# Performance work log

Hardware: AMD Instinct MI355X
Metric: run time of the kernel (lower is better)

Reference implementation:

```python
import jax, jax.numpy as jnp
import numpy as np

ALPHA = 0.1
B, N, M = 384, 256, 64
EPS = 1e-5


def _lsa(cost):
    """Exact linear sum assignment (Jonker-Volgenant shortest augmenting path).
    cost: (n, m) with n <= m. Returns col4row: for each row, its assigned column.
    Matches scipy.optimize.linear_sum_assignment.
    """
    cost = np.asarray(cost, dtype=np.float64)
    n, m = cost.shape
    u = np.zeros(n)
    v = np.zeros(m)
    col4row = np.full(n, -1, dtype=np.int64)
    row4col = np.full(m, -1, dtype=np.int64)
    for cur_row in range(n):
        min_val = 0.0
        i = cur_row
        SR = np.zeros(n, dtype=bool)
        SC = np.zeros(m, dtype=bool)
        shortest = np.full(m, np.inf)
        prev = np.full(m, -1, dtype=np.int64)
        sink = -1
        while sink == -1:
            SR[i] = True
            rem = ~SC
            cols = np.nonzero(rem)[0]
            d = min_val + cost[i, cols] - u[i] - v[cols]
            upd = d < shortest[cols]
            shortest[cols[upd]] = d[upd]
            prev[cols[upd]] = i
            j = int(np.argmin(np.where(SC, np.inf, shortest)))
            min_val = shortest[j]
            SC[j] = True
            if row4col[j] == -1:
                sink = j
            else:
                i = row4col[j]
        # dual updates
        u[cur_row] += min_val
        sr = SR.copy()
        sr[cur_row] = False
        rows = np.nonzero(sr)[0]
        u[rows] += min_val - shortest[col4row[rows]]
        scc = np.nonzero(SC)[0]
        v[scc] -= min_val - shortest[scc]
        # augment along the alternating path
        j = sink
        while True:
            i = prev[j]
            row4col[j] = i
            col4row[i], j = j, col4row[i]
            if i == cur_row:
                break
    return col4row


def _assignments(pred_np, label_np, lens_np):
    """Build the (detached) one-hot assignment tensor X[b, pred, label]."""
    conf = pred_np[..., 3]
    log_c = np.log(conf + EPS)
    log_ca = np.log(1.0 - conf + EPS)
    X = np.zeros((pred_np.shape[0], pred_np.shape[1], label_np.shape[1]), dtype=np.float32)
    for b in range(pred_np.shape[0]):
        L = int(lens_np[b])
        diff = pred_np[b, :, None, :3] - label_np[b, None, :L, :]   # [N, L, 3]
        nd = (diff * diff).sum(-1)                                  # [N, L]
        C = ALPHA * nd / 2.0 - log_c[b][:, None] + log_ca[b][:, None]
        matched_preds = _lsa(C.T)                                   # [L] distinct pred indices
        X[b, matched_preds, np.arange(L)] = 1.0
    return X


def setup_inputs() -> dict:
    key = jax.random.key(0)
    k1, k2, k3 = jax.random.split(key, 3)
    pred = jax.random.uniform(k1, (B, N, 4), dtype=jnp.float32)      # coords + confidence in (0,1)
    label = jax.random.uniform(k2, (B, M, 3), dtype=jnp.float32)
    label_len = jax.random.randint(k3, (B,), 1, M + 1, dtype=jnp.int32)
    return {"pred": pred, "label": label, "label_len": label_len}


def reference(pred, label, label_len):
    # Host-side exact bipartite matching (detached, as in the torch original).
    X = jnp.asarray(_assignments(np.asarray(pred), np.asarray(label), np.asarray(label_len)))  # [B,N,M]
    x_c = 1.0 - X.sum(-1)                                   # [B,N] 1 for unmatched preds

    diff = pred[:, :, None, :3] - label[:, None, :, :]      # [B,N,M,3]
    normed = jnp.sum(diff * diff, axis=-1)                  # [B,N,M] squared L2
    conf = pred[:, :, 3]
    log_c = jnp.log(conf + EPS)
    log_ca = jnp.log(1.0 - conf + EPS)

    location_loss = jnp.sum(normed * X) / 2.0
    conf_pos_b = -jnp.einsum('bnm,bn->b', X, log_c)         # -(log_c_exp * X).sum per batch
    conf_neg_b = -jnp.sum(log_ca * x_c, axis=1)             # -(log_c_anti * x_c).sum per batch
    confidence_loss = jnp.sum(conf_pos_b + conf_neg_b + 1e-4)

    loss = ALPHA * location_loss + confidence_loss
    # Original returns last-batch confidence terms as diagnostics.
    return loss, ALPHA * location_loss, conf_pos_b[-1], conf_neg_b[-1]
```

## Files before the change

kernel.cpp:

```cpp
#include <hip/hip_runtime.h>
#include <math.h>


#define B_ 384
#define N_ 256
#define M_ 64

typedef unsigned long long u64;
typedef unsigned int u32;

#define WOFF   (1 << 20)
#define DCLAMP 0x007FFFFE
#define BIGF   3.0e8f
#define THF    1.0e8f

static __device__ __forceinline__ float readlane_f32(float x, int l) {
  return __int_as_float(__builtin_amdgcn_readlane(__float_as_int(x), l));
}

static __device__ __forceinline__ int qcost(float px_, float py_, float pz_,
                                            float base_,
                                            float lx, float ly, float lz) {
  const float t1 = __fmul_rn(px_, lx);
  const float t2 = __fmaf_rn(py_, ly, t1);
  const float t3 = __fmaf_rn(pz_, lz, t2);
  return (int)__fmaf_rn(t3, -3276.8f, base_);
}

static __device__ __forceinline__ void wave_min2_u32(u32& a, u32& b) {
  asm("s_nop 1\n\t"
      "v_min_u32_dpp %0, %0, %0 row_shr:1 row_mask:0xf bank_mask:0xf\n\t"
      "v_min_u32_dpp %1, %1, %1 row_shr:1 row_mask:0xf bank_mask:0xf\n\t"
      "v_min_u32_dpp %0, %0, %0 row_shr:2 row_mask:0xf bank_mask:0xf\n\t"
      "v_min_u32_dpp %1, %1, %1 row_shr:2 row_mask:0xf bank_mask:0xf\n\t"
      "v_min_u32_dpp %0, %0, %0 row_shr:4 row_mask:0xf bank_mask:0xf\n\t"
      "v_min_u32_dpp %1, %1, %1 row_shr:4 row_mask:0xf bank_mask:0xf\n\t"
      "v_min_u32_dpp %0, %0, %0 row_shr:8 row_mask:0xf bank_mask:0xf\n\t"
      "v_min_u32_dpp %1, %1, %1 row_shr:8 row_mask:0xf bank_mask:0xf\n\t"
      "v_min_u32_dpp %0, %0, %0 row_bcast:15 row_mask:0xa bank_mask:0xf\n\t"
      "v_min_u32_dpp %1, %1, %1 row_bcast:15 row_mask:0xa bank_mask:0xf\n\t"
      "v_min_u32_dpp %0, %0, %0 row_bcast:31 row_mask:0xc bank_mask:0xf\n\t"
      "v_min_u32_dpp %1, %1, %1 row_bcast:31 row_mask:0xc bank_mask:0xf"
      : "+v"(a), "+v"(b));
}

__global__ __launch_bounds__(64) void lsa_loss_kernel(
    const float* __restrict__ pred,
    const float* __restrict__ label,
    const int* __restrict__ label_len,
    double* __restrict__ ws,
    float* __restrict__ out)
{
  const int b = blockIdx.x;
  const int lane = threadIdx.x;

  __shared__ float lab_x[M_], lab_y[M_], lab_z[M_];
  __shared__ int r4c_lds[N_];

  const float* lp = label + (size_t)(b * M_ + lane) * 3;
  const float labx = lp[0], laby = lp[1], labz = lp[2];
  lab_x[lane] = labx; lab_y[lane] = laby; lab_z[lane] = labz;

  float px[4], py[4], pz[4], lc[4], lca[4], base[4], baseO[4], baseB[4];
  int v[4];
  u32 jc[4];
  const float4* pred4 = reinterpret_cast<const float4*>(pred);
#pragma unroll
  for (int k = 0; k < 4; ++k) {
    const float4 p = pred4[b * N_ + lane + 64 * k];
    px[k] = p.x; py[k] = p.y; pz[k] = p.z;
    lc[k]  = logf(__fadd_rn(p.w, 1e-5f));
    lca[k] = logf(__fadd_rn(__fsub_rn(1.0f, p.w), 1e-5f));
    const float qgf = __fmul_rn(__fsub_rn(lca[k], lc[k]), 32768.0f);
    const float npp = __fmaf_rn(p.z, p.z, __fmaf_rn(p.y, p.y, __fmul_rn(p.x, p.x)));
    base[k]  = __fmaf_rn(npp, 1638.4f, qgf);
    baseO[k] = base[k];
    baseB[k] = base[k] + BIGF;
    v[k] = 0;
    jc[k] = (u32)(lane + 64 * k);
  }
  int c4r = -1;
  int u_reg = 0;

  int L = label_len[b];
  L = (L < 1) ? 1 : ((L > M_) ? M_ : L);

  __syncthreads();

  for (int r = 0; r < L; ++r) {
    const float lx = readlane_f32(labx, r);
    const float ly = readlane_f32(laby, r);
    const float lz = readlane_f32(labz, r);
    u32 cand[4];
#pragma unroll
    for (int k = 0; k < 4; ++k) {
      const int q = qcost(px[k], py[k], pz[k], base[k], lx, ly, lz);
      cand[k] = ((u32)(q + WOFF) << 8) | jc[k];
    }
    u32 ca = (cand[0] < cand[1]) ? cand[0] : cand[1];
    u32 cb = (cand[2] < cand[3]) ? cand[2] : cand[3];
    wave_min2_u32(ca, cb);
    const u32 wa = (u32)__builtin_amdgcn_readlane((int)ca, 63);
    const u32 wb = (u32)__builtin_amdgcn_readlane((int)cb, 63);
    const u32 wk = (wa < wb) ? wa : wb;
    const int j1 = (int)(wk & 0xFF);
    if (lane == r) u_reg = (int)(wk >> 8) - WOFF;
    const bool taken = __ballot(c4r == j1) != 0ull;
    if (!taken && lane == r) c4r = j1;
  }
  u64 free_mask = __ballot((lane < L) && (c4r < 0));

  while (free_mask) {
    const int cur_row = (int)__builtin_ctzll(free_mask);
    free_mask &= free_mask - 1;

    u32 shk[4] = {0x7FFFFFFFu, 0x7FFFFFFFu, 0x7FFFFFFFu, 0x7FFFFFFFu};
    int mvj = 0, joined = 0, min_val = 0;
    int i_cur = cur_row;
    int u_i = __builtin_amdgcn_readlane(u_reg, i_cur);
    float lx = readlane_f32(labx, i_cur);
    float ly = readlane_f32(laby, i_cur);
    float lz = readlane_f32(labz, i_cur);
    int t = 0 - u_i;
    int sink = -1;

    while (true) {
      u32 cand[4];
#pragma unroll
      for (int k = 0; k < 4; ++k) {
        const int tv = t - v[k];
        int dd = qcost(px[k], py[k], pz[k], base[k], lx, ly, lz) + tv;
        dd = (dd < DCLAMP) ? dd : DCLAMP;
        const u32 rkey = ((u32)dd << 8) | jc[k];
        const u32 skey = ((u32)dd << 8) | (u32)i_cur;
        shk[k] = (skey < shk[k]) ? skey : shk[k];
        cand[k] = rkey;
      }
      u32 ca = (cand[0] < cand[1]) ? cand[0] : cand[1];
      u32 cb = (cand[2] < cand[3]) ? cand[2] : cand[3];
      wave_min2_u32(ca, cb);
      const u32 wa = (u32)__builtin_amdgcn_readlane((int)ca, 63);
      const u32 wb = (u32)__builtin_amdgcn_readlane((int)cb, 63);
      const u32 wk = (wa < wb) ? wa : wb;
      const int j_min = (int)(wk & 0xFF);
      min_val = (int)(wk >> 8);
      const int kk = j_min >> 6;
      const bool selfc = (lane == (j_min & 63));
      base[0] = (selfc && kk == 0) ? baseB[0] : base[0];
      base[1] = (selfc && kk == 1) ? baseB[1] : base[1];
      base[2] = (selfc && kk == 2) ? baseB[2] : base[2];
      base[3] = (selfc && kk == 3) ? baseB[3] : base[3];
      const bool own = (c4r == j_min);
      const u64 om = __ballot(own);
      if (om == 0ull) { sink = j_min; break; }
      i_cur = (int)__builtin_ctzll(om);
      if (own) { mvj = min_val; joined = 1; }
      u_i = __builtin_amdgcn_readlane(u_reg, i_cur);
      lx = readlane_f32(labx, i_cur);
      ly = readlane_f32(laby, i_cur);
      lz = readlane_f32(labz, i_cur);
      t = min_val - u_i;
    }

    if (lane == cur_row)  u_reg += min_val;
    else if (joined)      u_reg += min_val - mvj;
#pragma unroll
    for (int k = 0; k < 4; ++k) {
      if (base[k] > THF) {
        v[k] -= (min_val - (int)(shk[k] >> 8));
        base[k] = baseO[k];
      }
    }

    {
      int j = sink;
      while (true) {
        const int kkj = j >> 6, lj = j & 63;
        const int s0 = __builtin_amdgcn_readlane((int)shk[0], lj);
        const int s1 = __builtin_amdgcn_readlane((int)shk[1], lj);
        const int s2 = __builtin_amdgcn_readlane((int)shk[2], lj);
        const int s3 = __builtin_amdgcn_readlane((int)shk[3], lj);
        const int ps = (kkj == 0) ? s0 : (kkj == 1) ? s1 : (kkj == 2) ? s2 : s3;
        const int ii = ps & 0xFF;
        const int jn = __builtin_amdgcn_readlane(c4r, ii);
        if (lane == ii) c4r = j;
        if (ii == cur_row) break;
        j = jn;
      }
    }
  }

#pragma unroll
  for (int k = 0; k < 4; ++k) r4c_lds[lane + 64 * k] = -1;
  __syncthreads();
  if (c4r >= 0) r4c_lds[c4r] = lane;
  __syncthreads();

  double loc = 0.0, cpos = 0.0, cneg = 0.0;
#pragma unroll
  for (int k = 0; k < 4; ++k) {
    const int l = r4c_lds[lane + 64 * k];
    if (l >= 0) {
      const float d0 = __fsub_rn(px[k], lab_x[l]);
      const float d1 = __fsub_rn(py[k], lab_y[l]);
      const float d2 = __fsub_rn(pz[k], lab_z[l]);
      const float nd = __fadd_rn(__fadd_rn(__fmul_rn(d0, d0), __fmul_rn(d1, d1)),
                                 __fmul_rn(d2, d2));
      loc += (double)nd;
      cpos -= (double)lc[k];
    } else {
      cneg -= (double)lca[k];
    }
  }
  for (int off = 32; off >= 1; off >>= 1) {
    loc += __shfl_xor(loc, off, 64);
    cpos += __shfl_xor(cpos, off, 64);
    cneg += __shfl_xor(cneg, off, 64);
  }

  if (lane == 0) {
    atomicAdd(&ws[0], loc);
    atomicAdd(&ws[1], cpos + cneg + 1e-4);
    if (b == B_ - 1) { atomicAdd(&ws[2], cpos); atomicAdd(&ws[3], cneg); }
    __threadfence();
    unsigned int* cnt = (unsigned int*)(ws + 4);
    const unsigned int old = atomicAdd(cnt, 1u);
    if (old == (unsigned int)(B_ - 1)) {
      __threadfence();
      const double loc_t  = atomicAdd(&ws[0], 0.0);
      const double conf_t = atomicAdd(&ws[1], 0.0);
      const double cpos_l = atomicAdd(&ws[2], 0.0);
      const double cneg_l = atomicAdd(&ws[3], 0.0);
      const double lloc = 0.1 * (loc_t * 0.5);
      out[0] = (float)(lloc + conf_t);
      out[1] = (float)lloc;
      out[2] = (float)cpos_l;
      out[3] = (float)cneg_l;
    }
  }
}

extern "C" void kernel_launch(void* const* d_in, const int* in_sizes, int n_in,
                              void* d_out, int out_size, void* d_ws, size_t ws_size,
                              hipStream_t stream) {
  const float* pred = (const float*)d_in[0];
  const float* label = (const float*)d_in[1];
  const int* label_len = (const int*)d_in[2];
  double* ws = (double*)d_ws;
  float* out = (float*)d_out;

  hipMemsetAsync(d_ws, 0, 64, stream);
  lsa_loss_kernel<<<B_, 64, 0, stream>>>(pred, label, label_len, ws, out);
}
```

Baseline: 153.2 us.

## Replace greedy init with two-pass auction-style augmenting row reduction

The greedy column-reduction initialisation becomes an auction / augmenting-row-reduction pass. Each row finds its best and second-best reduced cost using a top-2 wave reduction. It lowers the winning column's price by the gap plus an epsilon, steals the column from its previous owner, and requeues that owner for a second pass. The aim is to leave fewer free rows for the expensive shortest-augmenting-path phase. The cost is a wider per-row reduction, and epsilon-perturbed duals could interact with exactness of the later JV phase.

```diff
diff --git a/kernel.cpp b/kernel.cpp
--- a/kernel.cpp
+++ b/kernel.cpp
@@ -13,6 +13,7 @@
 #define DCLAMP 0x007FFFFE
 #define BIGF   3.0e8f
 #define THF    1.0e8f
+#define EPSQ   64
 
 static __device__ __forceinline__ float readlane_f32(float x, int l) {
   return __int_as_float(__builtin_amdgcn_readlane(__float_as_int(x), l));
@@ -44,6 +45,16 @@
       : "+v"(a), "+v"(b));
 }
 
+#define MIN2_STEP(CTRL, RMASK)                                                 \
+  {                                                                            \
+    const u32 n1 = (u32)__builtin_amdgcn_update_dpp(-1, (int)m1, CTRL, RMASK, 0xF, false); \
+    const u32 n2 = (u32)__builtin_amdgcn_update_dpp(-1, (int)m2, CTRL, RMASK, 0xF, false); \
+    const u32 mx = (m1 > n1) ? m1 : n1;                                        \
+    m1 = (m1 < n1) ? m1 : n1;                                                  \
+    const u32 mn2 = (m2 < n2) ? m2 : n2;                                       \
+    m2 = (mn2 < mx) ? mn2 : mx;                                                \
+  }
+
 __global__ __launch_bounds__(64) void lsa_loss_kernel(
     const float* __restrict__ pred,
     const float* __restrict__ label,
@@ -87,26 +98,57 @@
 
   __syncthreads();
 
-  for (int r = 0; r < L; ++r) {
-    const float lx = readlane_f32(labx, r);
-    const float ly = readlane_f32(laby, r);
-    const float lz = readlane_f32(labz, r);
-    u32 cand[4];
-#pragma unroll
-    for (int k = 0; k < 4; ++k) {
-      const int q = qcost(px[k], py[k], pz[k], base[k], lx, ly, lz);
-      cand[k] = ((u32)(q + WOFF) << 8) | jc[k];
-    }
-    u32 ca = (cand[0] < cand[1]) ? cand[0] : cand[1];
-    u32 cb = (cand[2] < cand[3]) ? cand[2] : cand[3];
-    wave_min2_u32(ca, cb);
-    const u32 wa = (u32)__builtin_amdgcn_readlane((int)ca, 63);
-    const u32 wb = (u32)__builtin_amdgcn_readlane((int)cb, 63);
-    const u32 wk = (wa < wb) ? wa : wb;
-    const int j1 = (int)(wk & 0xFF);
-    if (lane == r) u_reg = (int)(wk >> 8) - WOFF;
-    const bool taken = __ballot(c4r == j1) != 0ull;
-    if (!taken && lane == r) c4r = j1;
+  u64 pend = (L >= 64) ? ~0ull : ((1ull << L) - 1ull);
+  for (int pass = 0; pass < 2; ++pass) {
+    u64 next = 0ull;
+    while (pend) {
+      const int r = (int)__builtin_ctzll(pend);
+      pend &= pend - 1ull;
+      const float lx = readlane_f32(labx, r);
+      const float ly = readlane_f32(laby, r);
+      const float lz = readlane_f32(labz, r);
+      u32 cand[4];
+#pragma unroll
+      for (int k = 0; k < 4; ++k) {
+        const int q = (qcost(px[k], py[k], pz[k], base[k], lx, ly, lz) - v[k]) + WOFF;
+        cand[k] = ((u32)q << 8) | jc[k];
+      }
+      const u32 lo01 = (cand[0] < cand[1]) ? cand[0] : cand[1];
+      const u32 hi01 = (cand[0] < cand[1]) ? cand[1] : cand[0];
+      const u32 lo23 = (cand[2] < cand[3]) ? cand[2] : cand[3];
+      const u32 hi23 = (cand[2] < cand[3]) ? cand[3] : cand[2];
+      u32 m1 = (lo01 < lo23) ? lo01 : lo23;
+      const u32 mxl = (lo01 < lo23) ? lo23 : lo01;
+      const u32 mnh = (hi01 < hi23) ? hi01 : hi23;
+      u32 m2 = (mnh < mxl) ? mnh : mxl;
+      MIN2_STEP(0x111, 0xF);
+      MIN2_STEP(0x112, 0xF);
+      MIN2_STEP(0x114, 0xF);
+      MIN2_STEP(0x118, 0xF);
+      MIN2_STEP(0x142, 0xA);
+      MIN2_STEP(0x143, 0xC);
+      const u32 w1 = (u32)__builtin_amdgcn_readlane((int)m1, 63);
+      const u32 w2 = (u32)__builtin_amdgcn_readlane((int)m2, 63);
+      const int j1 = (int)(w1 & 0xFF);
+      const int d1 = (int)(w1 >> 8);
+      const int d2 = (int)(w2 >> 8);
+      if (lane == r) u_reg = d2 - WOFF;
+      const int vdec = (d2 - d1) + EPSQ;
+      const int kk1 = j1 >> 6;
+      const bool selfc = (lane == (j1 & 63));
+      v[0] -= (selfc && kk1 == 0) ? vdec : 0;
+      v[1] -= (selfc && kk1 == 1) ? vdec : 0;
+      v[2] -= (selfc && kk1 == 2) ? vdec : 0;
+      v[3] -= (selfc && kk1 == 3) ? vdec : 0;
+      const u64 om = __ballot(c4r == j1);
+      if (om != 0ull) {
+        const int kold = (int)__builtin_ctzll(om);
+        next |= (1ull << kold);
+        if (lane == kold) c4r = -1;
+      }
+      if (lane == r) c4r = j1;
+    }
+    pend = next;
   }
   u64 free_mask = __ballot((lane < L) && (c4r < 0));
 
```

New measurement: 170.7 us. +11.4%, slower.

## Initialize column duals from column minima to speed up the assignment warm start

Applied to the files above, without the earlier changes.

Adds a pass that computes, per prediction column, the minimum quantized cost over all labels. A threshold theta is then found by bisection so that roughly L-8 columns fall below it, and column duals v are set to min(mcol-theta, 0). The greedy initial row assignment then uses reduced costs (cost - v), which should yield more non-conflicting initial matches and fewer shortest-augmenting-path iterations. The price is an extra pass over all labels plus about 21 ballot iterations per block. It also risks overflow or range issues in the packed 24-bit key if reduced costs exceed the WOFF bounds.

```diff
diff --git a/kernel.cpp b/kernel.cpp
--- a/kernel.cpp
+++ b/kernel.cpp
@@ -87,6 +87,36 @@
 
   __syncthreads();
 
+  int mcol[4] = {0x7FFFFFFF, 0x7FFFFFFF, 0x7FFFFFFF, 0x7FFFFFFF};
+  for (int r = 0; r < L; ++r) {
+    const float lx = readlane_f32(labx, r);
+    const float ly = readlane_f32(laby, r);
+    const float lz = readlane_f32(labz, r);
+#pragma unroll
+    for (int k = 0; k < 4; ++k) {
+      const int q = qcost(px[k], py[k], pz[k], base[k], lx, ly, lz);
+      mcol[k] = (q < mcol[k]) ? q : mcol[k];
+    }
+  }
+  {
+    const int R = (L > 9) ? (L - 8) : 1;
+    int lo = -(1 << 20), hi = (1 << 20);
+    while (hi - lo > 1) {
+      const int mid = lo + ((hi - lo) >> 1);
+      const int cnt = __popcll(__ballot(mcol[0] < mid))
+                    + __popcll(__ballot(mcol[1] < mid))
+                    + __popcll(__ballot(mcol[2] < mid))
+                    + __popcll(__ballot(mcol[3] < mid));
+      if (cnt <= R) lo = mid; else hi = mid;
+    }
+    const int theta = lo;
+#pragma unroll
+    for (int k = 0; k < 4; ++k) {
+      const int vc = mcol[k] - theta;
+      v[k] = (vc < 0) ? vc : 0;
+    }
+  }
+
   for (int r = 0; r < L; ++r) {
     const float lx = readlane_f32(labx, r);
     const float ly = readlane_f32(laby, r);
@@ -94,8 +124,8 @@
     u32 cand[4];
 #pragma unroll
     for (int k = 0; k < 4; ++k) {
-      const int q = qcost(px[k], py[k], pz[k], base[k], lx, ly, lz);
-      cand[k] = ((u32)(q + WOFF) << 8) | jc[k];
+      const int q = (qcost(px[k], py[k], pz[k], base[k], lx, ly, lz) - v[k]) + WOFF;
+      cand[k] = ((u32)q << 8) | jc[k];
     }
     u32 ca = (cand[0] < cand[1]) ? cand[0] : cand[1];
     u32 cb = (cand[2] < cand[3]) ? cand[2] : cand[3];
```

Result: slower. 181.2 us (+18.2%).
